# Optimization experiments

Measured on AMD Instinct MI355X. Metric: run time of the kernel, lower is better.

## Reference

```python
import jax, jax.numpy as jnp
import numpy as np

D_K = 64.0  # key size from init


def setup_inputs() -> dict:
    key = jax.random.key(0)
    k1, k2, k3, k4, k5 = jax.random.split(key, 5)
    B, H, S, D = 2, 16, 2048, 64
    q = jax.random.normal(k1, (B, H, S, D), dtype=jnp.float32)
    v = jax.random.normal(k2, (B, H, S, D), dtype=jnp.float32)
    k = jax.random.normal(k3, (B, H, S, D), dtype=jnp.float32)
    att_mask = jax.random.normal(k4, (B, 1, S, S), dtype=jnp.float32)
    seq_mask = jax.random.uniform(k5, (B, 1, 1, S), dtype=jnp.float32)
    return {"q": q, "v": v, "k": k, "att_mask": att_mask, "seq_mask": seq_mask}


def reference(q, v, k, att_mask, seq_mask):
    # scores: [B, H, S, S]
    scores = jnp.einsum("bhqd,bhkd->bhqk", q, k) / jnp.sqrt(jnp.asarray(D_K, q.dtype))
    scores = scores + att_mask
    weights = jax.nn.softmax(scores, axis=-1)
    weights = weights * seq_mask  # post-softmax mask, no renormalization
    out = jnp.einsum("bhqk,bhkd->bhqd", weights, v)
    return out
```

## Files before the change

### kernel.cpp

```cpp
#include <hip/hip_runtime.h>
#include <hip/hip_bf16.h>
#include <stdint.h>

typedef __attribute__((ext_vector_type(8)))  short    short8;
typedef __attribute__((ext_vector_type(4)))  float    floatx4;
typedef __attribute__((ext_vector_type(16))) float    floatx16;
typedef __attribute__((ext_vector_type(2)))  uint32_t uintx2;

static __device__ __forceinline__ uint32_t cvtpk(float lo, float hi) {
  uint32_t r;
  asm("v_cvt_pk_bf16_f32 %0, %1, %2" : "=v"(r) : "v"(lo), "v"(hi));
  return r;
}

static __device__ __forceinline__ short8 pack8c(floatx4 a, floatx4 b) {
  union { uint32_t u[4]; short8 s; } r;
  r.u[0] = cvtpk(a[0], a[1]); r.u[1] = cvtpk(a[2], a[3]);
  r.u[2] = cvtpk(b[0], b[1]); r.u[3] = cvtpk(b[2], b[3]);
  return r.s;
}

#define MFMA32(a, b, c) __builtin_amdgcn_mfma_f32_32x32x16_bf16((a), (b), (c), 0, 0, 0)

#define TILE_BARRIER() asm volatile("s_waitcnt lgkmcnt(0)\n\ts_barrier" ::: "memory")

constexpr int S_LEN = 2048;
constexpr int DH    = 64;
constexpr int QBLK  = 128;
constexpr int KVBLK = 64;
constexpr int NT    = S_LEN / KVBLK;

static __device__ __forceinline__ void swap32(uint32_t& a, uint32_t& b, int hi) {
#if __has_builtin(__builtin_amdgcn_permlane32_swap)
  typedef int intx2 __attribute__((ext_vector_type(2)));
  intx2 r = __builtin_amdgcn_permlane32_swap((int)a, (int)b, false, false);
  a = (uint32_t)r[0]; b = (uint32_t)r[1];
#else
  uint32_t pa = (uint32_t)__shfl_xor((int)a, 32, 64);
  uint32_t pb = (uint32_t)__shfl_xor((int)b, 32, 64);
  uint32_t na = hi ? pb : a;
  uint32_t nb = hi ? b  : pa;
  a = na; b = nb;
#endif
}

__global__ __launch_bounds__(256, 2)
void attn_fwd(const float* __restrict__ Q, const float* __restrict__ V,
              const float* __restrict__ K, const float* __restrict__ AM,
              const float* __restrict__ SM, float* __restrict__ O)
{
  __shared__ ushort Kl[2][KVBLK * DH];
  __shared__ ushort Vt[2][DH * KVBLK];
  __shared__ float  smlds[S_LEN];

  const int bh   = blockIdx.x;
  const int qt   = blockIdx.y;
  const int tid  = threadIdx.x;
  const int lane = tid & 63;
  const int wave = tid >> 6;
  const int l31  = lane & 31;
  const int hi   = lane >> 5;

  const float* qptr  = Q  + (size_t)bh * S_LEN * DH;
  const float* kptr  = K  + (size_t)bh * S_LEN * DH;
  const float* vptr  = V  + (size_t)bh * S_LEN * DH;
  const float* amptr = AM + (size_t)(bh >> 4) * S_LEN * S_LEN;
  const float* smptr = SM + (size_t)(bh >> 4) * S_LEN;
  float* optr = O + (size_t)bh * S_LEN * DH;

  for (int i = tid; i < S_LEN / 4; i += 256)
    ((floatx4*)smlds)[i] = ((const floatx4*)smptr)[i];

  const int qw = qt * QBLK + wave * 32;

  short8 qf[4];
  {
    const float* p = qptr + (size_t)(qw + l31) * DH + hi * 8;
    #pragma unroll
    for (int s = 0; s < 4; ++s) {
      floatx4 f0 = *(const floatx4*)(p + s * 16);
      floatx4 f1 = *(const floatx4*)(p + s * 16 + 4);
      qf[s] = pack8c(f0, f1);
    }
  }

  const int krow = tid >> 2;
  const int kcol = (tid & 3) * 16;
  const int kcb  = (tid & 3) * 2;
  const int vr0  = (tid & 15) * 4;
  const int vd0  = (tid >> 4) * 4;

  floatx4 kreg[4], vreg[4];
  floatx4 amA[2][4], amB[2][4];

  auto LOADKV = [&](int t) {
    const float* kg = kptr + (size_t)(t * KVBLK + krow) * DH + kcol;
    #pragma unroll
    for (int j = 0; j < 4; ++j) kreg[j] = ((const floatx4*)kg)[j];
    #pragma unroll
    for (int i = 0; i < 4; ++i)
      vreg[i] = *(const floatx4*)(vptr + (size_t)(t * KVBLK + vr0 + i) * DH + vd0);
  };

  auto WRITEKV = [&](int c) {
    const int sw = krow & 7;
    *(short8*)&Kl[c][krow * 64 + ((kcb ^ sw) * 8)]       = pack8c(kreg[0], kreg[1]);
    *(short8*)&Kl[c][krow * 64 + (((kcb + 1) ^ sw) * 8)] = pack8c(kreg[2], kreg[3]);
    #pragma unroll
    for (int d = 0; d < 4; ++d) {
      uintx2 w;
      w[0] = cvtpk(vreg[0][d], vreg[1][d]);
      w[1] = cvtpk(vreg[2][d], vreg[3][d]);
      const int row = vd0 + d;
      const int ch  = (vr0 >> 3) ^ (row & 7);
      *(uintx2*)&Vt[c][row * 64 + ch * 8 + (vr0 & 7)] = w;
    }
  };

  auto LOADAM = [&](int t, floatx4 (&am)[2][4]) {
    const float* base = amptr + (size_t)(qw + l31) * S_LEN + t * KVBLK + hi * 4;
    #pragma unroll
    for (int blk = 0; blk < 2; ++blk)
      #pragma unroll
      for (int j = 0; j < 4; ++j)
        am[blk][j] = *(const floatx4*)(base + blk * 32 + j * 8);
  };

  LOADKV(0);
  WRITEKV(0);
  LOADAM(0, amA);
  TILE_BARRIER();

  float m_run = -3.0e38f, l_run = 0.f;
  floatx16 oacc[2];
  #pragma unroll
  for (int db = 0; db < 2; ++db)
    #pragma unroll
    for (int r = 0; r < 16; ++r) oacc[db][r] = 0.f;

  auto STEP = [&](int t, int c, floatx4 (&amC)[2][4], floatx4 (&amN)[2][4]) {
    floatx16 sacc[2];
    __builtin_amdgcn_s_setprio(1);
    #pragma unroll
    for (int blk = 0; blk < 2; ++blk) {
      #pragma unroll
      for (int r = 0; r < 16; ++r) sacc[blk][r] = 0.f;
      const int row = blk * 32 + l31;
      const int sw  = row & 7;
      #pragma unroll
      for (int s = 0; s < 4; ++s) {
        const int ch = (s * 2 + hi) ^ sw;
        short8 kf = *(const short8*)&Kl[c][row * 64 + ch * 8];
        sacc[blk] = MFMA32(kf, qf[s], sacc[blk]);
      }
    }
    __builtin_amdgcn_s_setprio(0);

    const int tn = (t + 1 < NT) ? t + 1 : NT - 1;
    LOADKV(tn);
    LOADAM(tn, amN);

    float p[2][16];
    float pmax = -3.0e38f;
    #pragma unroll
    for (int blk = 0; blk < 2; ++blk)
      #pragma unroll
      for (int r = 0; r < 16; ++r) {
        const float v = fmaf(sacc[blk][r], 0.125f, amC[blk][r >> 2][r & 3]);
        p[blk][r] = v;
        pmax = fmaxf(pmax, v);
      }
    pmax = fmaxf(pmax, __shfl_xor(pmax, 32, 64));

    if (__any(pmax > m_run)) {
      const float mnew = fmaxf(m_run, pmax);
      const float fac  = __expf(m_run - mnew);
      float fw[16];
      #pragma unroll
      for (int r = 0; r < 16; ++r)
        fw[r] = __shfl(fac, (r & 3) + 8 * (r >> 2) + 4 * hi, 64);
      #pragma unroll
      for (int db = 0; db < 2; ++db)
        #pragma unroll
        for (int r = 0; r < 16; ++r) oacc[db][r] *= fw[r];
      l_run *= fac;
      m_run = mnew;
    }

    float ssum = 0.f;
    #pragma unroll
    for (int blk = 0; blk < 2; ++blk)
      #pragma unroll
      for (int r = 0; r < 16; ++r) {
        const float e = __expf(p[blk][r] - m_run);
        p[blk][r] = e;
        ssum += e;
      }
    ssum += __shfl_xor(ssum, 32, 64);
    l_run += ssum;

    floatx4 smv[2][4];
    #pragma unroll
    for (int blk = 0; blk < 2; ++blk)
      #pragma unroll
      for (int j = 0; j < 4; ++j)
        smv[blk][j] = *(const floatx4*)&smlds[t * KVBLK + blk * 32 + hi * 4 + j * 8];

    uint32_t pw[2][2][4];
    #pragma unroll
    for (int blk = 0; blk < 2; ++blk)
      #pragma unroll
      for (int ks = 0; ks < 2; ++ks) {
        uint32_t w0 = cvtpk(p[blk][ks * 8 + 0] * smv[blk][ks * 2 + 0][0],
                            p[blk][ks * 8 + 1] * smv[blk][ks * 2 + 0][1]);
        uint32_t w1 = cvtpk(p[blk][ks * 8 + 2] * smv[blk][ks * 2 + 0][2],
                            p[blk][ks * 8 + 3] * smv[blk][ks * 2 + 0][3]);
        uint32_t w2 = cvtpk(p[blk][ks * 8 + 4] * smv[blk][ks * 2 + 1][0],
                            p[blk][ks * 8 + 5] * smv[blk][ks * 2 + 1][1]);
        uint32_t w3 = cvtpk(p[blk][ks * 8 + 6] * smv[blk][ks * 2 + 1][2],
                            p[blk][ks * 8 + 7] * smv[blk][ks * 2 + 1][3]);
        swap32(w0, w2, hi);
        swap32(w1, w3, hi);
        pw[blk][ks][0] = w0; pw[blk][ks][1] = w1;
        pw[blk][ks][2] = w2; pw[blk][ks][3] = w3;
      }

    __builtin_amdgcn_s_setprio(1);
    #pragma unroll
    for (int blk = 0; blk < 2; ++blk)
      #pragma unroll
      for (int ks = 0; ks < 2; ++ks) {
        union { uint32_t u[4]; short8 s; } af;
        af.u[0] = pw[blk][ks][0]; af.u[1] = pw[blk][ks][1];
        af.u[2] = pw[blk][ks][2]; af.u[3] = pw[blk][ks][3];
        #pragma unroll
        for (int db = 0; db < 2; ++db) {
          const int row = db * 32 + l31;
          const int ch  = (blk * 4 + ks * 2 + hi) ^ (row & 7);
          short8 vf = *(const short8*)&Vt[c][row * 64 + ch * 8];
          oacc[db] = MFMA32(af.s, vf, oacc[db]);
        }
      }
    __builtin_amdgcn_s_setprio(0);

    WRITEKV(c ^ 1);
    TILE_BARRIER();
  };

  #pragma unroll 1
  for (int t = 0; t < NT; t += 2) {
    STEP(t,     0, amA, amB);
    STEP(t + 1, 1, amB, amA);
  }

  const float inv = 1.0f / l_run;
  float iw[16];
  #pragma unroll
  for (int r = 0; r < 16; ++r)
    iw[r] = __shfl(inv, (r & 3) + 8 * (r >> 2) + 4 * hi, 64);
  #pragma unroll
  for (int db = 0; db < 2; ++db)
    #pragma unroll
    for (int r = 0; r < 16; ++r) {
      const int qr = (r & 3) + 8 * (r >> 2) + 4 * hi;
      optr[(size_t)(qw + qr) * DH + db * 32 + l31] = oacc[db][r] * iw[r];
    }
}

extern "C" void kernel_launch(void* const* d_in, const int* in_sizes, int n_in,
                              void* d_out, int out_size, void* d_ws, size_t ws_size,
                              hipStream_t stream) {
  const float* q  = (const float*)d_in[0];
  const float* v  = (const float*)d_in[1];
  const float* k  = (const float*)d_in[2];
  const float* am = (const float*)d_in[3];
  const float* sm = (const float*)d_in[4];
  float* o = (float*)d_out;

  dim3 grid(32, S_LEN / QBLK);
  attn_fwd<<<grid, 256, 0, stream>>>(q, v, k, am, sm, o);
}
```

Baseline: 121.3 us.

## Split KV range across two blocks with a combine kernel (flash-decoding style)

Adds a split-KV mode in which each query tile is processed by two blocks, each covering half of the key/value sequence. Each block writes its unnormalized partial output plus running max and sum, and a second kernel merges the two halves with log-sum-exp rescaling. This doubles the grid from 512 to 1024 blocks to raise GPU occupancy. Launch bounds go from 2 to 4 blocks per CU, and the seq_mask LDS copy is dropped in favour of direct global reads. In exchange it adds an extra kernel launch, extra global traffic for the partial outputs, and register pressure from the tighter launch bound.

```diff
diff --git a/kernel.cpp b/kernel.cpp
--- a/kernel.cpp
+++ b/kernel.cpp
@@ -29,6 +29,7 @@
 constexpr int QBLK  = 128;
 constexpr int KVBLK = 64;
 constexpr int NT    = S_LEN / KVBLK;
+constexpr size_t NROWS = 32 * (size_t)S_LEN;
 
 static __device__ __forceinline__ void swap32(uint32_t& a, uint32_t& b, int hi) {
 #if __has_builtin(__builtin_amdgcn_permlane32_swap)
@@ -44,17 +45,23 @@
 #endif
 }
 
-__global__ __launch_bounds__(256, 2)
+template<bool SPLIT>
+__global__ __launch_bounds__(256, 4)
 void attn_fwd(const float* __restrict__ Q, const float* __restrict__ V,
               const float* __restrict__ K, const float* __restrict__ AM,
-              const float* __restrict__ SM, float* __restrict__ O)
+              const float* __restrict__ SM, float* __restrict__ O,
+              float* __restrict__ PO1, float* __restrict__ PM, float* __restrict__ PL)
 {
   __shared__ ushort Kl[2][KVBLK * DH];
   __shared__ ushort Vt[2][DH * KVBLK];
-  __shared__ float  smlds[S_LEN];
 
   const int bh   = blockIdx.x;
   const int qt   = blockIdx.y;
+  const int kvh  = SPLIT ? blockIdx.z : 0;
+  const int NT_LOC = SPLIT ? NT / 2 : NT;
+  const int t0   = kvh * NT_LOC;
+  const int tlast = t0 + NT_LOC - 1;
+
   const int tid  = threadIdx.x;
   const int lane = tid & 63;
   const int wave = tid >> 6;
@@ -66,10 +73,6 @@
   const float* vptr  = V  + (size_t)bh * S_LEN * DH;
   const float* amptr = AM + (size_t)(bh >> 4) * S_LEN * S_LEN;
   const float* smptr = SM + (size_t)(bh >> 4) * S_LEN;
-  float* optr = O + (size_t)bh * S_LEN * DH;
-
-  for (int i = tid; i < S_LEN / 4; i += 256)
-    ((floatx4*)smlds)[i] = ((const floatx4*)smptr)[i];
 
   const int qw = qt * QBLK + wave * 32;
 
@@ -126,9 +129,9 @@
         am[blk][j] = *(const floatx4*)(base + blk * 32 + j * 8);
   };
 
-  LOADKV(0);
+  LOADKV(t0);
   WRITEKV(0);
-  LOADAM(0, amA);
+  LOADAM(t0, amA);
   TILE_BARRIER();
 
   float m_run = -3.0e38f, l_run = 0.f;
@@ -138,7 +141,7 @@
     #pragma unroll
     for (int r = 0; r < 16; ++r) oacc[db][r] = 0.f;
 
-  auto STEP = [&](int t, int c, floatx4 (&amC)[2][4], floatx4 (&amN)[2][4]) {
+  auto STEP = [&](int tt, int c, floatx4 (&amC)[2][4], floatx4 (&amN)[2][4]) {
     floatx16 sacc[2];
     __builtin_amdgcn_s_setprio(1);
     #pragma unroll
@@ -156,7 +159,7 @@
     }
     __builtin_amdgcn_s_setprio(0);
 
-    const int tn = (t + 1 < NT) ? t + 1 : NT - 1;
+    const int tn = (tt < tlast) ? tt + 1 : tlast;
     LOADKV(tn);
     LOADAM(tn, amN);
 
@@ -204,7 +207,7 @@
     for (int blk = 0; blk < 2; ++blk)
       #pragma unroll
       for (int j = 0; j < 4; ++j)
-        smv[blk][j] = *(const floatx4*)&smlds[t * KVBLK + blk * 32 + hi * 4 + j * 8];
+        smv[blk][j] = *(const floatx4*)(smptr + tt * KVBLK + blk * 32 + hi * 4 + j * 8);
 
     uint32_t pw[2][2][4];
     #pragma unroll
@@ -248,23 +251,58 @@
   };
 
   #pragma unroll 1
-  for (int t = 0; t < NT; t += 2) {
-    STEP(t,     0, amA, amB);
-    STEP(t + 1, 1, amB, amA);
+  for (int t = 0; t < NT_LOC; t += 2) {
+    STEP(t0 + t,     0, amA, amB);
+    STEP(t0 + t + 1, 1, amB, amA);
   }
 
-  const float inv = 1.0f / l_run;
-  float iw[16];
-  #pragma unroll
-  for (int r = 0; r < 16; ++r)
-    iw[r] = __shfl(inv, (r & 3) + 8 * (r >> 2) + 4 * hi, 64);
-  #pragma unroll
-  for (int db = 0; db < 2; ++db)
-    #pragma unroll
-    for (int r = 0; r < 16; ++r) {
-      const int qr = (r & 3) + 8 * (r >> 2) + 4 * hi;
-      optr[(size_t)(qw + qr) * DH + db * 32 + l31] = oacc[db][r] * iw[r];
-    }
+  if (SPLIT) {
+    float* po = (kvh == 0) ? O : PO1;
+    po += (size_t)bh * S_LEN * DH;
+    #pragma unroll
+    for (int db = 0; db < 2; ++db)
+      #pragma unroll
+      for (int r = 0; r < 16; ++r) {
+        const int qr = (r & 3) + 8 * (r >> 2) + 4 * hi;
+        po[(size_t)(qw + qr) * DH + db * 32 + l31] = oacc[db][r];
+      }
+    if (hi == 0) {
+      const size_t ri = (size_t)kvh * NROWS + (size_t)bh * S_LEN + qw + l31;
+      PM[ri] = m_run;
+      PL[ri] = l_run;
+    }
+  } else {
+    float* optr = O + (size_t)bh * S_LEN * DH;
+    const float inv = 1.0f / l_run;
+    float iw[16];
+    #pragma unroll
+    for (int r = 0; r < 16; ++r)
+      iw[r] = __shfl(inv, (r & 3) + 8 * (r >> 2) + 4 * hi, 64);
+    #pragma unroll
+    for (int db = 0; db < 2; ++db)
+      #pragma unroll
+      for (int r = 0; r < 16; ++r) {
+        const int qr = (r & 3) + 8 * (r >> 2) + 4 * hi;
+        optr[(size_t)(qw + qr) * DH + db * 32 + l31] = oacc[db][r] * iw[r];
+      }
+  }
+}
+
+__global__ __launch_bounds__(256)
+void attn_combine(const float* __restrict__ PO1, const float* __restrict__ PM,
+                  const float* __restrict__ PL, float* __restrict__ O)
+{
+  const size_t idx = (size_t)blockIdx.x * 256 + threadIdx.x;
+  const size_t row = idx >> 4;
+  const float m0 = PM[row], m1 = PM[NROWS + row];
+  const float l0 = PL[row], l1 = PL[NROWS + row];
+  const float m  = fmaxf(m0, m1);
+  const float f0 = __expf(m0 - m);
+  const float f1 = __expf(m1 - m);
+  const float inv = 1.0f / (l0 * f0 + l1 * f1);
+  floatx4 a = ((const floatx4*)O)[idx];
+  floatx4 b = ((const floatx4*)PO1)[idx];
+  ((floatx4*)O)[idx] = (a * f0 + b * f1) * inv;
 }
 
 extern "C" void kernel_launch(void* const* d_in, const int* in_sizes, int n_in,
@@ -277,6 +315,20 @@
   const float* sm = (const float*)d_in[4];
   float* o = (float*)d_out;
 
-  dim3 grid(32, S_LEN / QBLK);
-  attn_fwd<<<grid, 256, 0, stream>>>(q, v, k, am, sm, o);
-}
+  const size_t po1_f = NROWS * DH;
+  const size_t ml_f  = 2 * NROWS;
+  const size_t need  = (po1_f + 2 * ml_f) * sizeof(float);
+
+  if (ws_size >= need) {
+    float* po1 = (float*)d_ws;
+    float* pm  = po1 + po1_f;
+    float* pl  = pm + ml_f;
+    dim3 grid(32, S_LEN / QBLK, 2);
+    attn_fwd<true><<<grid, 256, 0, stream>>>(q, v, k, am, sm, o, po1, pm, pl);
+    attn_combine<<<(NROWS * DH / 4) / 256, 256, 0, stream>>>(po1, pm, pl, o);
+  } else {
+    dim3 grid(32, S_LEN / QBLK, 1);
+    attn_fwd<false><<<grid, 256, 0, stream>>>(q, v, k, am, sm, o,
+                                              nullptr, nullptr, nullptr);
+  }
+}
```

Result: slower. 460.6 us (+279.7%).

## Prefetch K/V two tiles ahead, single-buffer att_mask, read seq_mask from global

Applied to the files above, without the earlier changes.

K/V global loads now go into two alternating register sets, so each tile is fetched two steps before it is written to LDS. This gives the loads a full iteration of latency hiding. The att_mask prefetch drops to a single register set that is reloaded after the scores are computed. The seq_mask LDS staging is removed and values are read straight from global memory each step. Together this rebalances register pressure and LDS use, but the extra K/V registers may hurt occupancy at 2 blocks per CU, and the direct seq_mask loads add global latency inside the softmax path.

```diff
diff --git a/kernel.cpp b/kernel.cpp
--- a/kernel.cpp
+++ b/kernel.cpp
@@ -51,10 +51,10 @@
 {
   __shared__ ushort Kl[2][KVBLK * DH];
   __shared__ ushort Vt[2][DH * KVBLK];
-  __shared__ float  smlds[S_LEN];
 
   const int bh   = blockIdx.x;
   const int qt   = blockIdx.y;
+
   const int tid  = threadIdx.x;
   const int lane = tid & 63;
   const int wave = tid >> 6;
@@ -68,9 +68,6 @@
   const float* smptr = SM + (size_t)(bh >> 4) * S_LEN;
   float* optr = O + (size_t)bh * S_LEN * DH;
 
-  for (int i = tid; i < S_LEN / 4; i += 256)
-    ((floatx4*)smlds)[i] = ((const floatx4*)smptr)[i];
-
   const int qw = qt * QBLK + wave * 32;
 
   short8 qf[4];
@@ -90,10 +87,10 @@
   const int vr0  = (tid & 15) * 4;
   const int vd0  = (tid >> 4) * 4;
 
-  floatx4 kreg[4], vreg[4];
-  floatx4 amA[2][4], amB[2][4];
-
-  auto LOADKV = [&](int t) {
+  floatx4 kregA[4], vregA[4], kregB[4], vregB[4];
+  floatx4 amx[2][4];
+
+  auto LOADKV = [&](int t, floatx4 (&kreg)[4], floatx4 (&vreg)[4]) {
     const float* kg = kptr + (size_t)(t * KVBLK + krow) * DH + kcol;
     #pragma unroll
     for (int j = 0; j < 4; ++j) kreg[j] = ((const floatx4*)kg)[j];
@@ -102,7 +99,7 @@
       vreg[i] = *(const floatx4*)(vptr + (size_t)(t * KVBLK + vr0 + i) * DH + vd0);
   };
 
-  auto WRITEKV = [&](int c) {
+  auto WRITEKV = [&](int c, floatx4 (&kreg)[4], floatx4 (&vreg)[4]) {
     const int sw = krow & 7;
     *(short8*)&Kl[c][krow * 64 + ((kcb ^ sw) * 8)]       = pack8c(kreg[0], kreg[1]);
     *(short8*)&Kl[c][krow * 64 + (((kcb + 1) ^ sw) * 8)] = pack8c(kreg[2], kreg[3]);
@@ -117,18 +114,19 @@
     }
   };
 
-  auto LOADAM = [&](int t, floatx4 (&am)[2][4]) {
+  auto LOADAM = [&](int t) {
     const float* base = amptr + (size_t)(qw + l31) * S_LEN + t * KVBLK + hi * 4;
     #pragma unroll
     for (int blk = 0; blk < 2; ++blk)
       #pragma unroll
       for (int j = 0; j < 4; ++j)
-        am[blk][j] = *(const floatx4*)(base + blk * 32 + j * 8);
-  };
-
-  LOADKV(0);
-  WRITEKV(0);
-  LOADAM(0, amA);
+        amx[blk][j] = *(const floatx4*)(base + blk * 32 + j * 8);
+  };
+
+  LOADKV(0, kregA, vregA);
+  WRITEKV(0, kregA, vregA);
+  LOADKV(1, kregB, vregB);
+  LOADAM(0);
   TILE_BARRIER();
 
   float m_run = -3.0e38f, l_run = 0.f;
@@ -138,39 +136,46 @@
     #pragma unroll
     for (int r = 0; r < 16; ++r) oacc[db][r] = 0.f;
 
-  auto STEP = [&](int t, int c, floatx4 (&amC)[2][4], floatx4 (&amN)[2][4]) {
-    floatx16 sacc[2];
+  auto STEP = [&](int tt, int c,
+                  floatx4 (&kW)[4], floatx4 (&vW)[4],
+                  floatx4 (&kL)[4], floatx4 (&vL)[4]) {
+    floatx16 sc[2];
     __builtin_amdgcn_s_setprio(1);
     #pragma unroll
     for (int blk = 0; blk < 2; ++blk) {
       #pragma unroll
-      for (int r = 0; r < 16; ++r) sacc[blk][r] = 0.f;
+      for (int r = 0; r < 16; ++r) sc[blk][r] = 0.f;
       const int row = blk * 32 + l31;
       const int sw  = row & 7;
       #pragma unroll
       for (int s = 0; s < 4; ++s) {
         const int ch = (s * 2 + hi) ^ sw;
         short8 kf = *(const short8*)&Kl[c][row * 64 + ch * 8];
-        sacc[blk] = MFMA32(kf, qf[s], sacc[blk]);
+        sc[blk] = MFMA32(kf, qf[s], sc[blk]);
       }
     }
     __builtin_amdgcn_s_setprio(0);
 
-    const int tn = (t + 1 < NT) ? t + 1 : NT - 1;
-    LOADKV(tn);
-    LOADAM(tn, amN);
-
-    float p[2][16];
     float pmax = -3.0e38f;
     #pragma unroll
     for (int blk = 0; blk < 2; ++blk)
       #pragma unroll
       for (int r = 0; r < 16; ++r) {
-        const float v = fmaf(sacc[blk][r], 0.125f, amC[blk][r >> 2][r & 3]);
-        p[blk][r] = v;
+        const float v = fmaf(sc[blk][r], 0.125f, amx[blk][r >> 2][r & 3]);
+        sc[blk][r] = v;
         pmax = fmaxf(pmax, v);
       }
     pmax = fmaxf(pmax, __shfl_xor(pmax, 32, 64));
+
+    const int tn = (tt + 1 < NT) ? tt + 1 : NT - 1;
+    LOADAM(tn);
+
+    floatx4 smv[2][4];
+    #pragma unroll
+    for (int blk = 0; blk < 2; ++blk)
+      #pragma unroll
+      for (int j = 0; j < 4; ++j)
+        smv[blk][j] = *(const floatx4*)(smptr + tt * KVBLK + blk * 32 + hi * 4 + j * 8);
 
     if (__any(pmax > m_run)) {
       const float mnew = fmaxf(m_run, pmax);
@@ -192,33 +197,26 @@
     for (int blk = 0; blk < 2; ++blk)
       #pragma unroll
       for (int r = 0; r < 16; ++r) {
-        const float e = __expf(p[blk][r] - m_run);
-        p[blk][r] = e;
+        const float e = __expf(sc[blk][r] - m_run);
+        sc[blk][r] = e;
         ssum += e;
       }
     ssum += __shfl_xor(ssum, 32, 64);
     l_run += ssum;
 
-    floatx4 smv[2][4];
-    #pragma unroll
-    for (int blk = 0; blk < 2; ++blk)
-      #pragma unroll
-      for (int j = 0; j < 4; ++j)
-        smv[blk][j] = *(const floatx4*)&smlds[t * KVBLK + blk * 32 + hi * 4 + j * 8];
-
     uint32_t pw[2][2][4];
     #pragma unroll
     for (int blk = 0; blk < 2; ++blk)
       #pragma unroll
       for (int ks = 0; ks < 2; ++ks) {
-        uint32_t w0 = cvtpk(p[blk][ks * 8 + 0] * smv[blk][ks * 2 + 0][0],
-                            p[blk][ks * 8 + 1] * smv[blk][ks * 2 + 0][1]);
-        uint32_t w1 = cvtpk(p[blk][ks * 8 + 2] * smv[blk][ks * 2 + 0][2],
-                            p[blk][ks * 8 + 3] * smv[blk][ks * 2 + 0][3]);
-        uint32_t w2 = cvtpk(p[blk][ks * 8 + 4] * smv[blk][ks * 2 + 1][0],
-                            p[blk][ks * 8 + 5] * smv[blk][ks * 2 + 1][1]);
-        uint32_t w3 = cvtpk(p[blk][ks * 8 + 6] * smv[blk][ks * 2 + 1][2],
-                            p[blk][ks * 8 + 7] * smv[blk][ks * 2 + 1][3]);
+        uint32_t w0 = cvtpk(sc[blk][ks * 8 + 0] * smv[blk][ks * 2 + 0][0],
+                            sc[blk][ks * 8 + 1] * smv[blk][ks * 2 + 0][1]);
+        uint32_t w1 = cvtpk(sc[blk][ks * 8 + 2] * smv[blk][ks * 2 + 0][2],
+                            sc[blk][ks * 8 + 3] * smv[blk][ks * 2 + 0][3]);
+        uint32_t w2 = cvtpk(sc[blk][ks * 8 + 4] * smv[blk][ks * 2 + 1][0],
+                            sc[blk][ks * 8 + 5] * smv[blk][ks * 2 + 1][1]);
+        uint32_t w3 = cvtpk(sc[blk][ks * 8 + 6] * smv[blk][ks * 2 + 1][2],
+                            sc[blk][ks * 8 + 7] * smv[blk][ks * 2 + 1][3]);
         swap32(w0, w2, hi);
         swap32(w1, w3, hi);
         pw[blk][ks][0] = w0; pw[blk][ks][1] = w1;
@@ -243,14 +241,16 @@
       }
     __builtin_amdgcn_s_setprio(0);
 
-    WRITEKV(c ^ 1);
+    WRITEKV(c ^ 1, kW, vW);
+    const int t2 = (tt + 2 < NT) ? tt + 2 : NT - 1;
+    LOADKV(t2, kL, vL);
     TILE_BARRIER();
   };
 
   #pragma unroll 1
   for (int t = 0; t < NT; t += 2) {
-    STEP(t,     0, amA, amB);
-    STEP(t + 1, 1, amB, amA);
+    STEP(t,     0, kregB, vregB, kregA, vregA);
+    STEP(t + 1, 1, kregA, vregA, kregB, vregB);
   }
 
   const float inv = 1.0f / l_run;
```

Result: slower. 143.4 us (+18.2%).
